# Optimization experiments

Measured on AMD Instinct MI355X. Metric: run time of the kernel, lower is better.

## Reference

```python
import jax, jax.numpy as jnp
import numpy as np

HIDDEN = 1024
HEADS = 16
HEAD_DIM = HIDDEN // HEADS
B, S = 2, 2048


def setup_inputs() -> dict:
    key = jax.random.key(0)
    k1, k2, k3 = jax.random.split(key, 3)
    scale_in = 1.0 / np.sqrt(HIDDEN)
    x = jax.random.normal(k1, (B, S, HIDDEN), dtype=jnp.float32)
    wqkv_w = jax.random.normal(k2, (3 * HIDDEN, HIDDEN), dtype=jnp.float32) * scale_in
    wo_w = jax.random.normal(k3, (HIDDEN, HIDDEN), dtype=jnp.float32) * scale_in
    wo_b = jnp.zeros((HIDDEN,), dtype=jnp.float32)
    return {"x": x, "wqkv_w": wqkv_w, "wo_w": wo_w, "wo_b": wo_b}


def reference(x, wqkv_w, wo_w, wo_b):
    b, s, d = x.shape
    h, hd = HEADS, HEAD_DIM
    sm_scale = hd ** (-0.5)
    # QKV projection (torch Linear: x @ W^T), then chunk into q,k,v
    qkv = jnp.einsum('bsd,ed->bse', x, wqkv_w)  # [b, s, 3d]
    q, k, v = jnp.split(qkv, 3, axis=-1)
    # [b, h, s, hd]
    q = q.reshape(b, s, h, hd).transpose(0, 2, 1, 3)
    k = k.reshape(b, s, h, hd).transpose(0, 2, 1, 3)
    v = v.reshape(b, s, h, hd).transpose(0, 2, 1, 3)
    # raw scores, then causal mask (mask applied BEFORE scaling, as in source;
    # -inf * scale == -inf so math matches softmax(score*scale) with mask)
    scores = jnp.einsum('bhqe,bhke->bhqk', q, k)
    causal = jnp.tril(jnp.ones((s, s), dtype=bool))
    scores = jnp.where(causal[None, None, :, :], scores, -jnp.inf)
    weights = jax.nn.softmax(scores * sm_scale, axis=-1)
    # dropout p=0.0 (eval) -> identity
    out = jnp.einsum('bhqk,bhke->bhqe', weights, v)
    out = out.transpose(0, 2, 1, 3).reshape(b, s, h * hd)
    y = jnp.einsum('bsd,ed->bse', out, wo_w) + wo_b
    return (y, k, v)
```

## Files before the change

kernel.cpp:

```cpp
#include <hip/hip_runtime.h>
#include <cstdint>
#include <cstddef>


using bf16x8 = __attribute__((ext_vector_type(8))) __bf16;
using f32x4  = __attribute__((ext_vector_type(4))) float;
using u16    = unsigned short;

#define SOFT_SCALE 0.1803368801111244f

__device__ __forceinline__ u16 f2bf(float f) {
  union { float f; uint32_t u; } a; a.f = f;
  uint32_t r = a.u + 0x7fffu + ((a.u >> 16) & 1u);
  return (u16)(r >> 16);
}

__device__ __forceinline__ bf16x8 ldfrag(const u16* p) {
  return *reinterpret_cast<const bf16x8*>(p);
}

__device__ __forceinline__ void gload_lds16(const void* g, void* l) {
  __builtin_amdgcn_global_load_lds((const __attribute__((address_space(1))) void*)g,
                                   (__attribute__((address_space(3))) void*)l,
                                   16, 0, 0);
}

__device__ __forceinline__ uint32_t cvt_pk_bf16(float a, float b) {
  uint32_t r;
  asm("v_cvt_pk_bf16_f32 %0, %1, %2" : "=v"(r) : "v"(a), "v"(b));
  return r;
}

__global__ void cvt_all(const float* __restrict__ x, const float* __restrict__ wqkv,
                        const float* __restrict__ wo,
                        u16* __restrict__ xb, u16* __restrict__ wqkvb, u16* __restrict__ wob) {
  int i = blockIdx.x * blockDim.x + threadIdx.x;
  int stride = gridDim.x * blockDim.x;
  for (; i < 2097152; i += stride) {
    const float* src; u16* dst; int j;
    if (i < 1048576)      { src = x;    dst = xb;    j = i; }
    else if (i < 1835008) { src = wqkv; dst = wqkvb; j = i - 1048576; }
    else                  { src = wo;   dst = wob;   j = i - 1835008; }
    float4 v = reinterpret_cast<const float4*>(src)[j];
    ushort4 o;
    o.x = f2bf(v.x); o.y = f2bf(v.y); o.z = f2bf(v.z); o.w = f2bf(v.w);
    reinterpret_cast<ushort4*>(dst)[j] = o;
  }
}

__global__ __launch_bounds__(512, 2) void qkv_gemm_kernel(
    const u16* __restrict__ Xb, const u16* __restrict__ Wb,
    u16* __restrict__ Qws, u16* __restrict__ Kws, u16* __restrict__ Vtws,
    float* __restrict__ out) {
  extern __shared__ char smem[];

  const int tid = threadIdx.x, lane = tid & 63, wid = tid >> 6;
  const int wr = wid >> 2, wc = wid & 3;
  const int fq = lane >> 4, fr = lane & 15;

  const int wg = (blockIdx.x & 7) * 64 + (blockIdx.x >> 3);
  const int bm = wg >> 4, bn = wg & 15;
  const int m0 = bm * 128, n0 = bn * 192;

  const char* Ab = (const char*)Xb + (size_t)m0 * 2048;
  const char* Bb = (const char*)Wb + (size_t)n0 * 2048;

  f32x4 acc[4][3] = {};

  auto stage_A = [&](int t, int h) {
    char* dst = smem + (t & 1) * 16384 + h * 8192;
    int lin = tid * 16;
    int rl  = lin >> 7;
    int col = (lin & 127) ^ ((rl & 7) << 4);
    gload_lds16(Ab + (size_t)(h * 64 + rl) * 2048 + t * 128 + col, dst + lin);
  };
  auto stage_B = [&](int t) {
    char* dst = smem + 32768 + (t & 1) * 24576;
#pragma unroll
    for (int l = 0; l < 3; ++l) {
      int lin = (l * 512 + tid) * 16;
      int rl  = lin >> 7;
      int col = (lin & 127) ^ ((rl & 7) << 4);
      gload_lds16(Bb + (size_t)rl * 2048 + t * 128 + col, dst + lin);
    }
  };

  stage_A(0, 0); stage_A(0, 1);
  stage_B(0);
  stage_B(1);
  asm volatile("s_waitcnt vmcnt(3)" ::: "memory");
  __builtin_amdgcn_s_barrier();

  bf16x8 afr[2][2];
  bf16x8 bfr[3][2];

  for (int t = 0; t < 16; ++t) {
    const char* As = smem + (t & 1) * 16384;
    const char* Bs = smem + 32768 + (t & 1) * 24576;

#pragma unroll
    for (int m = 0; m < 2; ++m) {
      int row = wr * 64 + m * 16 + fr;
#pragma unroll
      for (int ks = 0; ks < 2; ++ks)
        afr[m][ks] = *(const bf16x8*)(As + row * 128 + ((ks * 64 + fq * 16) ^ ((row & 7) << 4)));
    }
#pragma unroll
    for (int n = 0; n < 3; ++n) {
      int row = wc * 48 + n * 16 + fr;
#pragma unroll
      for (int ks = 0; ks < 2; ++ks)
        bfr[n][ks] = *(const bf16x8*)(Bs + row * 128 + ((ks * 64 + fq * 16) ^ ((row & 7) << 4)));
    }
    if (t + 1 < 16) stage_A(t + 1, 0);
    __builtin_amdgcn_s_barrier();
    asm volatile("s_waitcnt lgkmcnt(0)" ::: "memory");
    __builtin_amdgcn_sched_barrier(0);
    __builtin_amdgcn_s_setprio(1);
#pragma unroll
    for (int m = 0; m < 2; ++m)
#pragma unroll
      for (int n = 0; n < 3; ++n)
#pragma unroll
        for (int ks = 0; ks < 2; ++ks)
          acc[m][n] = __builtin_amdgcn_mfma_f32_16x16x32_bf16(afr[m][ks], bfr[n][ks], acc[m][n], 0, 0, 0);
    __builtin_amdgcn_s_setprio(0);
    __builtin_amdgcn_s_barrier();

#pragma unroll
    for (int m = 0; m < 2; ++m) {
      int row = wr * 64 + (m + 2) * 16 + fr;
#pragma unroll
      for (int ks = 0; ks < 2; ++ks)
        afr[m][ks] = *(const bf16x8*)(As + row * 128 + ((ks * 64 + fq * 16) ^ ((row & 7) << 4)));
    }
    if (t + 1 < 16) stage_A(t + 1, 1);
    if (t + 2 < 16) stage_B(t + 2);
    __builtin_amdgcn_s_barrier();
    asm volatile("s_waitcnt lgkmcnt(0)" ::: "memory");
    __builtin_amdgcn_sched_barrier(0);
    __builtin_amdgcn_s_setprio(1);
#pragma unroll
    for (int m = 0; m < 2; ++m)
#pragma unroll
      for (int n = 0; n < 3; ++n)
#pragma unroll
        for (int ks = 0; ks < 2; ++ks)
          acc[m + 2][n] = __builtin_amdgcn_mfma_f32_16x16x32_bf16(afr[m][ks], bfr[n][ks], acc[m + 2][n], 0, 0, 0);
    __builtin_amdgcn_s_setprio(0);
    if (t < 14)       asm volatile("s_waitcnt vmcnt(3)" ::: "memory");
    else if (t == 14) asm volatile("s_waitcnt vmcnt(0)" ::: "memory");
    __builtin_amdgcn_s_barrier();
  }

  const int mbase = m0 + wr * 64;
#pragma unroll
  for (int m = 0; m < 4; ++m)
#pragma unroll
    for (int n = 0; n < 3; ++n) {
      int mB = mbase + m * 16 + fq * 4;
      int ncol = n0 + wc * 48 + n * 16 + fr;
      int sect = ncol >> 10;
      int nn = ncol & 1023;
      int b = mB >> 11, s0 = mB & 2047;
      int h = nn >> 6, hd = nn & 63;
      size_t base = (((size_t)b * 16 + h) * 2048 + s0) * 64 + hd;
      float v0 = acc[m][n][0], v1 = acc[m][n][1], v2 = acc[m][n][2], v3 = acc[m][n][3];
      if (sect == 0) {
        Qws[base]       = f2bf(v0 * SOFT_SCALE);
        Qws[base + 64]  = f2bf(v1 * SOFT_SCALE);
        Qws[base + 128] = f2bf(v2 * SOFT_SCALE);
        Qws[base + 192] = f2bf(v3 * SOFT_SCALE);
      } else if (sect == 1) {
        Kws[base] = f2bf(v0); Kws[base + 64] = f2bf(v1);
        Kws[base + 128] = f2bf(v2); Kws[base + 192] = f2bf(v3);
        out[4194304 + base] = v0; out[4194304 + base + 64] = v1;
        out[4194304 + base + 128] = v2; out[4194304 + base + 192] = v3;
      } else {
        out[8388608 + base] = v0; out[8388608 + base + 64] = v1;
        out[8388608 + base + 128] = v2; out[8388608 + base + 192] = v3;
        size_t tt = ((size_t)(b * 16 + h) * 64 + hd) * 2048 + s0;
        ushort4 pk; pk.x = f2bf(v0); pk.y = f2bf(v1); pk.z = f2bf(v2); pk.w = f2bf(v3);
        *reinterpret_cast<ushort4*>(Vtws + tt) = pk;
      }
    }
}

__global__ __launch_bounds__(256, 4) void attn_kernel(
    const u16* __restrict__ Qw, const u16* __restrict__ Kw,
    const u16* __restrict__ Vtw, u16* __restrict__ Ow) {
  __shared__ u16 Ks[2][64 * 64];
  __shared__ u16 Vs[2][64 * 64];

  const int tid = threadIdx.x, lane = tid & 63, wid = tid >> 6;
  const int wk = wid >> 1, wh = wid & 1;
  const int fq = lane >> 4, fr = lane & 15;
  const int bh = blockIdx.x & 31;
  const int qb = 31 - (blockIdx.x >> 5);
  const int b = bh >> 4, h = bh & 15;
  const int q0 = qb * 64;

  const u16* Qbase  = Qw  + (size_t)bh * 2048 * 64;
  const u16* Kbase  = Kw  + (size_t)bh * 2048 * 64;
  const char* VtBase = (const char*)(Vtw + (size_t)bh * 64 * 2048);

#pragma unroll
  for (int f = 0; f < 2; ++f) {
    int lin = (f * 256 + tid) * 16;
    int row = lin >> 7;
    int logical = lin ^ ((row & 7) << 4);
    gload_lds16((const char*)Kbase + logical, (char*)Ks[0] + lin);
    gload_lds16(VtBase + (size_t)row * 4096 + (logical & 127), (char*)Vs[0] + lin);
  }

  bf16x8 qa[2][2];
#pragma unroll
  for (int qt = 0; qt < 2; ++qt)
#pragma unroll
    for (int kh = 0; kh < 2; ++kh)
      qa[qt][kh] = ldfrag(Qbase + (size_t)(q0 + wh * 32 + qt * 16 + fr) * 64 + kh * 32 + fq * 8);

  float ssum[2] = {0.f, 0.f};
  f32x4 accO[2][4] = {};

  int cur = 0;
  for (int kb = 0; kb <= qb; ++kb) {
    __syncthreads();

    if (kb < qb) {
      const char* kg = (const char*)(Kbase + (size_t)(kb + 1) * 64 * 64);
#pragma unroll
      for (int f = 0; f < 2; ++f) {
        int lin = (f * 256 + tid) * 16;
        int row = lin >> 7;
        int logical = lin ^ ((row & 7) << 4);
        gload_lds16(kg + logical, (char*)Ks[cur ^ 1] + lin);
        gload_lds16(VtBase + (size_t)row * 4096 + (size_t)(kb + 1) * 128 + (logical & 127),
                    (char*)Vs[cur ^ 1] + lin);
      }
    }

    const u16* Kc = Ks[cur];
    const u16* Vc = Vs[cur];

    f32x4 st[2][2];
    __builtin_amdgcn_s_setprio(1);
#pragma unroll
    for (int kvt = 0; kvt < 2; ++kvt) {
      int krow = wk * 32 + kvt * 16 + fr;
      bf16x8 kf0 = ldfrag(Kc + krow * 64 + ((fq * 8)      ^ ((krow & 7) << 3)));
      bf16x8 kf1 = ldfrag(Kc + krow * 64 + ((fq * 8 + 32) ^ ((krow & 7) << 3)));
#pragma unroll
      for (int qt = 0; qt < 2; ++qt) {
        f32x4 z = {};
        z = __builtin_amdgcn_mfma_f32_16x16x32_bf16(kf0, qa[qt][0], z, 0, 0, 0);
        z = __builtin_amdgcn_mfma_f32_16x16x32_bf16(kf1, qa[qt][1], z, 0, 0, 0);
        st[kvt][qt] = z;
      }
    }
    __builtin_amdgcn_s_setprio(0);

    uint32_t W[2][2][2];
#pragma unroll
    for (int qt = 0; qt < 2; ++qt) {
      int qrow = q0 + wh * 32 + qt * 16 + fr;
#pragma unroll
      for (int kvt = 0; kvt < 2; ++kvt) {
        float p0, p1, p2, p3;
        if (kb < qb) {
          p0 = exp2f(st[kvt][qt][0]);
          p1 = exp2f(st[kvt][qt][1]);
          p2 = exp2f(st[kvt][qt][2]);
          p3 = exp2f(st[kvt][qt][3]);
        } else {
          int kvg = kb * 64 + wk * 32 + kvt * 16 + fq * 4;
          p0 = (kvg + 0 > qrow) ? 0.f : exp2f(st[kvt][qt][0]);
          p1 = (kvg + 1 > qrow) ? 0.f : exp2f(st[kvt][qt][1]);
          p2 = (kvg + 2 > qrow) ? 0.f : exp2f(st[kvt][qt][2]);
          p3 = (kvg + 3 > qrow) ? 0.f : exp2f(st[kvt][qt][3]);
        }
        ssum[qt] += (p0 + p1) + (p2 + p3);
        W[qt][kvt][0] = cvt_pk_bf16(p0, p1);
        W[qt][kvt][1] = cvt_pk_bf16(p2, p3);
      }
    }

    union U { uint32_t u[4]; bf16x8 v; };
    U pa[2];
#pragma unroll
    for (int qt = 0; qt < 2; ++qt)
#pragma unroll
      for (int hh = 0; hh < 2; ++hh) {
        uint32_t a0 = W[qt][0][hh], b0 = W[qt][1][hh];
        asm("v_permlane32_swap_b32 %0, %1" : "+v"(a0), "+v"(b0));
        asm("v_permlane16_swap_b32 %0, %1" : "+v"(a0), "+v"(b0));
        pa[qt].u[hh] = a0; pa[qt].u[2 + hh] = b0;
      }

    __builtin_amdgcn_s_setprio(1);
#pragma unroll
    for (int ht = 0; ht < 4; ++ht) {
      int vrow = ht * 16 + fr;
      bf16x8 vb = ldfrag(Vc + vrow * 64 + ((wk * 32 + fq * 8) ^ ((vrow & 7) << 3)));
#pragma unroll
      for (int qt = 0; qt < 2; ++qt)
        accO[qt][ht] = __builtin_amdgcn_mfma_f32_16x16x32_bf16(pa[qt].v, vb, accO[qt][ht], 0, 0, 0);
    }
    __builtin_amdgcn_s_setprio(0);
    cur ^= 1;
  }

#pragma unroll
  for (int qt = 0; qt < 2; ++qt) {
    ssum[qt] += __shfl_xor(ssum[qt], 16);
    ssum[qt] += __shfl_xor(ssum[qt], 32);
  }

  __syncthreads();
  float* Ored = (float*)Ks;
  float* Sred = (float*)Vs;
  if (wk == 1) {
#pragma unroll
    for (int qt = 0; qt < 2; ++qt)
#pragma unroll
      for (int ht = 0; ht < 4; ++ht)
        *reinterpret_cast<f32x4*>(&Ored[(((wh * 2 + qt) * 4 + ht) << 8) + lane * 4]) = accO[qt][ht];
    if (fq == 0) {
      Sred[wh * 64 + fr]      = ssum[0];
      Sred[wh * 64 + 16 + fr] = ssum[1];
    }
  }
  __syncthreads();
  if (wk == 0) {
#pragma unroll
    for (int qt = 0; qt < 2; ++qt)
#pragma unroll
      for (int ht = 0; ht < 4; ++ht) {
        f32x4 o = *reinterpret_cast<const f32x4*>(&Ored[(((wh * 2 + qt) * 4 + ht) << 8) + lane * 4]);
        accO[qt][ht] += o;
      }
    float invq[2][4];
#pragma unroll
    for (int qt = 0; qt < 2; ++qt) {
      float s = ssum[qt] + Sred[wh * 64 + qt * 16 + fr];
      float inv = 1.0f / s;
#pragma unroll
      for (int r = 0; r < 4; ++r) invq[qt][r] = __shfl(inv, fq * 4 + r);
    }
#pragma unroll
    for (int qt = 0; qt < 2; ++qt)
#pragma unroll
      for (int ht = 0; ht < 4; ++ht)
#pragma unroll
        for (int r = 0; r < 4; ++r) {
          float o = accO[qt][ht][r] * invq[qt][r];
          int qr = q0 + wh * 32 + qt * 16 + fq * 4 + r;
          Ow[((size_t)b * 2048 + qr) * 1024 + h * 64 + ht * 16 + fr] = f2bf(o);
        }
  }
}

__global__ __launch_bounds__(512, 2) void proj_gemm_kernel(
    const u16* __restrict__ Ob, const u16* __restrict__ Wob,
    const float* __restrict__ bias, float* __restrict__ out) {
  extern __shared__ char smem[];

  const int tid = threadIdx.x, lane = tid & 63, wid = tid >> 6;
  const int wr = wid >> 2, wc = wid & 3;
  const int fq = lane >> 4, fr = lane & 15;

  const int wg = (blockIdx.x & 7) * 32 + (blockIdx.x >> 3);
  const int bm = wg >> 3, bn = wg & 7;
  const int m0 = bm * 128, n0 = bn * 128;

  const char* Ab = (const char*)Ob  + (size_t)m0 * 2048;
  const char* Bb = (const char*)Wob + (size_t)n0 * 2048;

  f32x4 acc[4][2] = {};

  auto stage = [&](int t, int mat, int h) {
    char* dst = smem + mat * 32768 + (t & 1) * 16384 + h * 8192;
    const char* src = mat ? Bb : Ab;
    int lin = tid * 16;
    int rl  = lin >> 7;
    int col = (lin & 127) ^ ((rl & 7) << 4);
    gload_lds16(src + (size_t)(h * 64 + rl) * 2048 + t * 128 + col, dst + lin);
  };

  stage(0, 0, 0); stage(0, 0, 1);
  stage(0, 1, 0); stage(0, 1, 1);
  stage(1, 1, 0); stage(1, 1, 1);
  asm volatile("s_waitcnt vmcnt(2)" ::: "memory");
  __builtin_amdgcn_s_barrier();

  bf16x8 afr[2][2];
  bf16x8 bfr[2][2];

  for (int t = 0; t < 16; ++t) {
    const char* As = smem + (t & 1) * 16384;
    const char* Bs = smem + 32768 + (t & 1) * 16384;

#pragma unroll
    for (int m = 0; m < 2; ++m) {
      int row = wr * 64 + m * 16 + fr;
#pragma unroll
      for (int ks = 0; ks < 2; ++ks)
        afr[m][ks] = *(const bf16x8*)(As + row * 128 + ((ks * 64 + fq * 16) ^ ((row & 7) << 4)));
    }
#pragma unroll
    for (int n = 0; n < 2; ++n) {
      int row = wc * 32 + n * 16 + fr;
#pragma unroll
      for (int ks = 0; ks < 2; ++ks)
        bfr[n][ks] = *(const bf16x8*)(Bs + row * 128 + ((ks * 64 + fq * 16) ^ ((row & 7) << 4)));
    }
    if (t + 1 < 16) stage(t + 1, 0, 0);
    __builtin_amdgcn_s_barrier();
    asm volatile("s_waitcnt lgkmcnt(0)" ::: "memory");
    __builtin_amdgcn_sched_barrier(0);
    __builtin_amdgcn_s_setprio(1);
#pragma unroll
    for (int m = 0; m < 2; ++m)
#pragma unroll
      for (int n = 0; n < 2; ++n)
#pragma unroll
        for (int ks = 0; ks < 2; ++ks)
          acc[m][n] = __builtin_amdgcn_mfma_f32_16x16x32_bf16(afr[m][ks], bfr[n][ks], acc[m][n], 0, 0, 0);
    __builtin_amdgcn_s_setprio(0);
    __builtin_amdgcn_s_barrier();

#pragma unroll
    for (int m = 0; m < 2; ++m) {
      int row = wr * 64 + (m + 2) * 16 + fr;
#pragma unroll
      for (int ks = 0; ks < 2; ++ks)
        afr[m][ks] = *(const bf16x8*)(As + row * 128 + ((ks * 64 + fq * 16) ^ ((row & 7) << 4)));
    }
    if (t + 1 < 16) stage(t + 1, 0, 1);
    if (t + 2 < 16) { stage(t + 2, 1, 0); stage(t + 2, 1, 1); }
    __builtin_amdgcn_s_barrier();
    asm volatile("s_waitcnt lgkmcnt(0)" ::: "memory");
    __builtin_amdgcn_sched_barrier(0);
    __builtin_amdgcn_s_setprio(1);
#pragma unroll
    for (int m = 0; m < 2; ++m)
#pragma unroll
      for (int n = 0; n < 2; ++n)
#pragma unroll
        for (int ks = 0; ks < 2; ++ks)
          acc[m + 2][n] = __builtin_amdgcn_mfma_f32_16x16x32_bf16(afr[m][ks], bfr[n][ks], acc[m + 2][n], 0, 0, 0);
    __builtin_amdgcn_s_setprio(0);
    if (t < 14)       asm volatile("s_waitcnt vmcnt(2)" ::: "memory");
    else if (t == 14) asm volatile("s_waitcnt vmcnt(0)" ::: "memory");
    __builtin_amdgcn_s_barrier();
  }

  const int mbase = m0 + wr * 64;
#pragma unroll
  for (int m = 0; m < 4; ++m)
#pragma unroll
    for (int n = 0; n < 2; ++n) {
      int mB = mbase + m * 16 + fq * 4;
      int ncol = n0 + wc * 32 + n * 16 + fr;
      float bv = bias[ncol];
#pragma unroll
      for (int r = 0; r < 4; ++r)
        out[(size_t)(mB + r) * 1024 + ncol] = acc[m][n][r] + bv;
    }
}

extern "C" void kernel_launch(void* const* d_in, const int* in_sizes, int n_in,
                              void* d_out, int out_size, void* d_ws, size_t ws_size,
                              hipStream_t stream) {
  const float* x    = (const float*)d_in[0];
  const float* wqkv = (const float*)d_in[1];
  const float* wo   = (const float*)d_in[2];
  const float* wo_b = (const float*)d_in[3];
  float* out = (float*)d_out;

  u16* xb    = (u16*)d_ws;
  u16* wqkvb = xb    + 4194304;
  u16* wob   = wqkvb + 3145728;
  u16* q_ws  = wob   + 1048576;
  u16* k_ws  = q_ws  + 4194304;
  u16* vt_ws = k_ws  + 4194304;
  u16* o_ws  = vt_ws + 4194304;

  static bool attr_set = false;
  if (!attr_set) {
    hipFuncSetAttribute((const void*)qkv_gemm_kernel,
                        hipFuncAttributeMaxDynamicSharedMemorySize, 131072);
    hipFuncSetAttribute((const void*)proj_gemm_kernel,
                        hipFuncAttributeMaxDynamicSharedMemorySize, 65536);
    attr_set = true;
  }

  cvt_all<<<2048, 256, 0, stream>>>(x, wqkv, wo, xb, wqkvb, wob);
  qkv_gemm_kernel<<<512, 512, 81920, stream>>>(xb, wqkvb, q_ws, k_ws, vt_ws, out);
  attn_kernel<<<32 * 32, 256, 0, stream>>>(q_ws, k_ws, vt_ws, o_ws);
  proj_gemm_kernel<<<256, 512, 65536, stream>>>(o_ws, wob, wo_b, out);
}
```

Before: 104.7 us.

## Process 128 query rows per attention block sharing staged K/V tiles

```diff
diff --git a/kernel.cpp b/kernel.cpp
--- a/kernel.cpp
+++ b/kernel.cpp
@@ -186,127 +186,125 @@
     }
 }
 
-__global__ __launch_bounds__(256, 4) void attn_kernel(
+__global__ __launch_bounds__(512, 4) void attn_kernel(
     const u16* __restrict__ Qw, const u16* __restrict__ Kw,
     const u16* __restrict__ Vtw, u16* __restrict__ Ow) {
-  __shared__ u16 Ks[2][64 * 64];
-  __shared__ u16 Vs[2][64 * 64];
+  __shared__ __align__(16) char sm[33280];
+  u16* Ks0 = (u16*)sm;
+  u16* Vs0 = (u16*)(sm + 16384);
+  float* Sred = (float*)(sm + 32768);
 
   const int tid = threadIdx.x, lane = tid & 63, wid = tid >> 6;
-  const int wk = wid >> 1, wh = wid & 1;
+  const int wh = wid >> 1, wk = wid & 1;
   const int fq = lane >> 4, fr = lane & 15;
   const int bh = blockIdx.x & 31;
-  const int qb = 31 - (blockIdx.x >> 5);
+  const int qb = 15 - (blockIdx.x >> 5);
   const int b = bh >> 4, h = bh & 15;
-  const int q0 = qb * 64;
+  const int q0 = qb * 128;
+  const int qwave = q0 + wh * 32;
 
   const u16* Qbase  = Qw  + (size_t)bh * 2048 * 64;
-  const u16* Kbase  = Kw  + (size_t)bh * 2048 * 64;
+  const char* Kbase = (const char*)(Kw + (size_t)bh * 2048 * 64);
   const char* VtBase = (const char*)(Vtw + (size_t)bh * 64 * 2048);
 
-#pragma unroll
-  for (int f = 0; f < 2; ++f) {
-    int lin = (f * 256 + tid) * 16;
+  auto stageKV = [&](int kt, int cc) {
+    int lin = tid * 16;
     int row = lin >> 7;
     int logical = lin ^ ((row & 7) << 4);
-    gload_lds16((const char*)Kbase + logical, (char*)Ks[0] + lin);
-    gload_lds16(VtBase + (size_t)row * 4096 + (logical & 127), (char*)Vs[0] + lin);
-  }
+    gload_lds16(Kbase + (size_t)kt * 8192 + logical, (char*)(Ks0 + cc * 4096) + lin);
+    gload_lds16(VtBase + (size_t)row * 4096 + (size_t)kt * 128 + (logical & 127),
+                (char*)(Vs0 + cc * 4096) + lin);
+  };
+
+  stageKV(0, 0);
 
   bf16x8 qa[2][2];
 #pragma unroll
   for (int qt = 0; qt < 2; ++qt)
 #pragma unroll
     for (int kh = 0; kh < 2; ++kh)
-      qa[qt][kh] = ldfrag(Qbase + (size_t)(q0 + wh * 32 + qt * 16 + fr) * 64 + kh * 32 + fq * 8);
+      qa[qt][kh] = ldfrag(Qbase + (size_t)(qwave + qt * 16 + fr) * 64 + kh * 32 + fq * 8);
 
   float ssum[2] = {0.f, 0.f};
   f32x4 accO[2][4] = {};
 
+  const int ktiles = 2 * qb + 2;
   int cur = 0;
-  for (int kb = 0; kb <= qb; ++kb) {
+  for (int kt = 0; kt < ktiles; ++kt) {
     __syncthreads();
 
-    if (kb < qb) {
-      const char* kg = (const char*)(Kbase + (size_t)(kb + 1) * 64 * 64);
-#pragma unroll
-      for (int f = 0; f < 2; ++f) {
-        int lin = (f * 256 + tid) * 16;
-        int row = lin >> 7;
-        int logical = lin ^ ((row & 7) << 4);
-        gload_lds16(kg + logical, (char*)Ks[cur ^ 1] + lin);
-        gload_lds16(VtBase + (size_t)row * 4096 + (size_t)(kb + 1) * 128 + (logical & 127),
-                    (char*)Vs[cur ^ 1] + lin);
+    if (kt + 1 < ktiles) stageKV(kt + 1, cur ^ 1);
+
+    if (kt * 64 <= qwave + 31) {
+      const u16* Kc = Ks0 + cur * 4096;
+      const u16* Vc = Vs0 + cur * 4096;
+
+      f32x4 st[2][2];
+      __builtin_amdgcn_s_setprio(1);
+#pragma unroll
+      for (int kvt = 0; kvt < 2; ++kvt) {
+        int krow = wk * 32 + kvt * 16 + fr;
+        bf16x8 kf0 = ldfrag(Kc + krow * 64 + ((fq * 8)      ^ ((krow & 7) << 3)));
+        bf16x8 kf1 = ldfrag(Kc + krow * 64 + ((fq * 8 + 32) ^ ((krow & 7) << 3)));
+#pragma unroll
+        for (int qt = 0; qt < 2; ++qt) {
+          f32x4 z = {};
+          z = __builtin_amdgcn_mfma_f32_16x16x32_bf16(kf0, qa[qt][0], z, 0, 0, 0);
+          z = __builtin_amdgcn_mfma_f32_16x16x32_bf16(kf1, qa[qt][1], z, 0, 0, 0);
+          st[kvt][qt] = z;
+        }
       }
-    }
-
-    const u16* Kc = Ks[cur];
-    const u16* Vc = Vs[cur];
-
-    f32x4 st[2][2];
-    __builtin_amdgcn_s_setprio(1);
-#pragma unroll
-    for (int kvt = 0; kvt < 2; ++kvt) {
-      int krow = wk * 32 + kvt * 16 + fr;
-      bf16x8 kf0 = ldfrag(Kc + krow * 64 + ((fq * 8)      ^ ((krow & 7) << 3)));
-      bf16x8 kf1 = ldfrag(Kc + krow * 64 + ((fq * 8 + 32) ^ ((krow & 7) << 3)));
+      __builtin_amdgcn_s_setprio(0);
+
+      const bool diag = (kt >= 2 * qb);
+      uint32_t W[2][2][2];
 #pragma unroll
       for (int qt = 0; qt < 2; ++qt) {
-        f32x4 z = {};
-        z = __builtin_amdgcn_mfma_f32_16x16x32_bf16(kf0, qa[qt][0], z, 0, 0, 0);
-        z = __builtin_amdgcn_mfma_f32_16x16x32_bf16(kf1, qa[qt][1], z, 0, 0, 0);
-        st[kvt][qt] = z;
+        int qrow = qwave + qt * 16 + fr;
+#pragma unroll
+        for (int kvt = 0; kvt < 2; ++kvt) {
+          float p0, p1, p2, p3;
+          if (!diag) {
+            p0 = exp2f(st[kvt][qt][0]);
+            p1 = exp2f(st[kvt][qt][1]);
+            p2 = exp2f(st[kvt][qt][2]);
+            p3 = exp2f(st[kvt][qt][3]);
+          } else {
+            int kvg = kt * 64 + wk * 32 + kvt * 16 + fq * 4;
+            p0 = (kvg + 0 > qrow) ? 0.f : exp2f(st[kvt][qt][0]);
+            p1 = (kvg + 1 > qrow) ? 0.f : exp2f(st[kvt][qt][1]);
+            p2 = (kvg + 2 > qrow) ? 0.f : exp2f(st[kvt][qt][2]);
+            p3 = (kvg + 3 > qrow) ? 0.f : exp2f(st[kvt][qt][3]);
+          }
+          ssum[qt] += (p0 + p1) + (p2 + p3);
+          W[qt][kvt][0] = cvt_pk_bf16(p0, p1);
+          W[qt][kvt][1] = cvt_pk_bf16(p2, p3);
+        }
       }
-    }
-    __builtin_amdgcn_s_setprio(0);
-
-    uint32_t W[2][2][2];
-#pragma unroll
-    for (int qt = 0; qt < 2; ++qt) {
-      int qrow = q0 + wh * 32 + qt * 16 + fr;
-#pragma unroll
-      for (int kvt = 0; kvt < 2; ++kvt) {
-        float p0, p1, p2, p3;
-        if (kb < qb) {
-          p0 = exp2f(st[kvt][qt][0]);
-          p1 = exp2f(st[kvt][qt][1]);
-          p2 = exp2f(st[kvt][qt][2]);
-          p3 = exp2f(st[kvt][qt][3]);
-        } else {
-          int kvg = kb * 64 + wk * 32 + kvt * 16 + fq * 4;
-          p0 = (kvg + 0 > qrow) ? 0.f : exp2f(st[kvt][qt][0]);
-          p1 = (kvg + 1 > qrow) ? 0.f : exp2f(st[kvt][qt][1]);
-          p2 = (kvg + 2 > qrow) ? 0.f : exp2f(st[kvt][qt][2]);
-          p3 = (kvg + 3 > qrow) ? 0.f : exp2f(st[kvt][qt][3]);
+
+      union U { uint32_t u[4]; bf16x8 v; };
+      U pa[2];
+#pragma unroll
+      for (int qt = 0; qt < 2; ++qt)
+#pragma unroll
+        for (int hh = 0; hh < 2; ++hh) {
+          uint32_t a0 = W[qt][0][hh], b0 = W[qt][1][hh];
+          asm("v_permlane32_swap_b32 %0, %1" : "+v"(a0), "+v"(b0));
+          asm("v_permlane16_swap_b32 %0, %1" : "+v"(a0), "+v"(b0));
+          pa[qt].u[hh] = a0; pa[qt].u[2 + hh] = b0;
         }
-        ssum[qt] += (p0 + p1) + (p2 + p3);
-        W[qt][kvt][0] = cvt_pk_bf16(p0, p1);
-        W[qt][kvt][1] = cvt_pk_bf16(p2, p3);
+
+      __builtin_amdgcn_s_setprio(1);
+#pragma unroll
+      for (int ht = 0; ht < 4; ++ht) {
+        int vrow = ht * 16 + fr;
+        bf16x8 vb = ldfrag(Vc + vrow * 64 + ((wk * 32 + fq * 8) ^ ((vrow & 7) << 3)));
+#pragma unroll
+        for (int qt = 0; qt < 2; ++qt)
+          accO[qt][ht] = __builtin_amdgcn_mfma_f32_16x16x32_bf16(pa[qt].v, vb, accO[qt][ht], 0, 0, 0);
       }
-    }
-
-    union U { uint32_t u[4]; bf16x8 v; };
-    U pa[2];
-#pragma unroll
-    for (int qt = 0; qt < 2; ++qt)
-#pragma unroll
-      for (int hh = 0; hh < 2; ++hh) {
-        uint32_t a0 = W[qt][0][hh], b0 = W[qt][1][hh];
-        asm("v_permlane32_swap_b32 %0, %1" : "+v"(a0), "+v"(b0));
-        asm("v_permlane16_swap_b32 %0, %1" : "+v"(a0), "+v"(b0));
-        pa[qt].u[hh] = a0; pa[qt].u[2 + hh] = b0;
-      }
-
-    __builtin_amdgcn_s_setprio(1);
-#pragma unroll
-    for (int ht = 0; ht < 4; ++ht) {
-      int vrow = ht * 16 + fr;
-      bf16x8 vb = ldfrag(Vc + vrow * 64 + ((wk * 32 + fq * 8) ^ ((vrow & 7) << 3)));
-#pragma unroll
-      for (int qt = 0; qt < 2; ++qt)
-        accO[qt][ht] = __builtin_amdgcn_mfma_f32_16x16x32_bf16(pa[qt].v, vb, accO[qt][ht], 0, 0, 0);
-    }
-    __builtin_amdgcn_s_setprio(0);
+      __builtin_amdgcn_s_setprio(0);
+    }
     cur ^= 1;
   }
 
@@ -317,8 +315,7 @@
   }
 
   __syncthreads();
-  float* Ored = (float*)Ks;
-  float* Sred = (float*)Vs;
+  float* Ored = (float*)sm;
   if (wk == 1) {
 #pragma unroll
     for (int qt = 0; qt < 2; ++qt)
@@ -326,8 +323,8 @@
       for (int ht = 0; ht < 4; ++ht)
         *reinterpret_cast<f32x4*>(&Ored[(((wh * 2 + qt) * 4 + ht) << 8) + lane * 4]) = accO[qt][ht];
     if (fq == 0) {
-      Sred[wh * 64 + fr]      = ssum[0];
-      Sred[wh * 64 + 16 + fr] = ssum[1];
+      Sred[wh * 32 + fr]      = ssum[0];
+      Sred[wh * 32 + 16 + fr] = ssum[1];
     }
   }
   __syncthreads();
@@ -342,7 +339,7 @@
     float invq[2][4];
 #pragma unroll
     for (int qt = 0; qt < 2; ++qt) {
-      float s = ssum[qt] + Sred[wh * 64 + qt * 16 + fr];
+      float s = ssum[qt] + Sred[wh * 32 + qt * 16 + fr];
       float inv = 1.0f / s;
 #pragma unroll
       for (int r = 0; r < 4; ++r) invq[qt][r] = __shfl(inv, fq * 4 + r);
@@ -354,7 +351,7 @@
 #pragma unroll
         for (int r = 0; r < 4; ++r) {
           float o = accO[qt][ht][r] * invq[qt][r];
-          int qr = q0 + wh * 32 + qt * 16 + fq * 4 + r;
+          int qr = qwave + qt * 16 + fq * 4 + r;
           Ow[((size_t)b * 2048 + qr) * 1024 + h * 64 + ht * 16 + fr] = f2bf(o);
         }
   }
@@ -497,6 +494,6 @@
 
   cvt_all<<<2048, 256, 0, stream>>>(x, wqkv, wo, xb, wqkvb, wob);
   qkv_gemm_kernel<<<512, 512, 81920, stream>>>(xb, wqkvb, q_ws, k_ws, vt_ws, out);
-  attn_kernel<<<32 * 32, 256, 0, stream>>>(q_ws, k_ws, vt_ws, o_ws);
+  attn_kernel<<<16 * 32, 512, 0, stream>>>(q_ws, k_ws, vt_ws, o_ws);
   proj_gemm_kernel<<<256, 512, 65536, stream>>>(o_ws, wob, wo_b, out);
 }
```

Result: no change. 105.4 us (+0.6%).
